# Kernel optimization log

Hardware: AMD Instinct MI355X
Metric: run time of the kernel (lower is better)

Reference implementation:

```python
import jax, jax.numpy as jnp
import numpy as np

E = 64      # embedding_dim
H = 64      # h_dim
MLP = 1024  # mlp_dim (attention hidden)
PRE1 = 512  # mlp_pre_pool hidden
BNK = 1024  # bottleneck_dim
S = 256     # num scenes (equal-size groups replacing seq_start_end)
P = 16      # pedestrians per scene
B = S * P   # total batch of pedestrians
T = 8       # obs_len for vx/vy (only last row used)
EPS = 1e-5  # BatchNorm eps


def _bn(x, g, b, m, v):
    # eval-mode BatchNorm1d over the last (feature) axis
    return (x - m) * jax.lax.rsqrt(v + EPS) * g + b


def setup_inputs() -> dict:
    key = jax.random.key(0)
    ks = jax.random.split(key, 24)
    def n(k, shape, s=1.0):
        return jax.random.normal(k, shape, jnp.float32) * s
    return {
        "h_states": n(ks[0], (1, B, H)),
        "end_pos": n(ks[1], (B, 2)),
        "vx": n(ks[2], (T, B)),
        "vy": n(ks[3], (T, B)),
        "W_sp": n(ks[4], (2, E), 0.05), "b_sp": jnp.zeros((E,), jnp.float32),
        "W_vel": n(ks[5], (2, E), 0.05), "b_vel": jnp.zeros((E,), jnp.float32),
        "Wa1": n(ks[6], (2 * E, MLP), 0.05), "ba1": jnp.zeros((MLP,), jnp.float32),
        "ga1": jnp.ones((MLP,), jnp.float32), "bta1": jnp.zeros((MLP,), jnp.float32),
        "ma1": n(ks[7], (MLP,), 0.1), "va1": jax.random.uniform(ks[8], (MLP,), jnp.float32) + 0.5,
        "Wa2": n(ks[9], (MLP, 1), 0.05), "ba2": jnp.zeros((1,), jnp.float32),
        "ga2": jnp.ones((1,), jnp.float32), "bta2": jnp.zeros((1,), jnp.float32),
        "ma2": n(ks[10], (1,), 0.1), "va2": jax.random.uniform(ks[11], (1,), jnp.float32) + 0.5,
        "Wp1": n(ks[12], (E + H, PRE1), 0.05), "bp1": jnp.zeros((PRE1,), jnp.float32),
        "gp1": jnp.ones((PRE1,), jnp.float32), "btp1": jnp.zeros((PRE1,), jnp.float32),
        "mp1": n(ks[13], (PRE1,), 0.1), "vp1": jax.random.uniform(ks[14], (PRE1,), jnp.float32) + 0.5,
        "Wp2": n(ks[15], (PRE1, BNK), 0.05), "bp2": jnp.zeros((BNK,), jnp.float32),
        "gp2": jnp.ones((BNK,), jnp.float32), "btp2": jnp.zeros((BNK,), jnp.float32),
        "mp2": n(ks[16], (BNK,), 0.1), "vp2": jax.random.uniform(ks[17], (BNK,), jnp.float32) + 0.5,
        "num_scenes": S, "num_ped": P,
    }


def _forward(h_states, end_pos, vx, vy, W_sp, b_sp, W_vel, b_vel,
             Wa1, ba1, ga1, bta1, ma1, va1, Wa2, ba2, ga2, bta2, ma2, va2,
             Wp1, bp1, gp1, btp1, mp1, vp1, Wp2, bp2, gp2, btp2, mp2, vp2,
             num_scenes, num_ped):
    Sn, Pn = num_scenes, num_ped
    h = h_states.reshape(-1, H).reshape(Sn, Pn, H)          # per-scene hidden
    pos = end_pos.reshape(Sn, Pn, 2)
    # rel[s,i,j] = pos[s,j] - pos[s,i]  (repeat vs repeat_interleave in torch)
    rel = pos[:, None, :, :] - pos[:, :, None, :]
    rel_emb = rel @ W_sp + b_sp                              # [S,P,P,E]
    vel = jnp.stack([vx[-1], vy[-1]], axis=-1).reshape(Sn, Pn, 2)
    vel_emb = vel @ W_vel + b_vel                            # [S,P,E], indexed by row i
    vel_emb = jnp.broadcast_to(vel_emb[:, :, None, :], (Sn, Pn, Pn, E))
    att_in = jnp.concatenate([rel_emb, vel_emb], axis=-1)    # [S,P,P,2E]
    a = jax.nn.relu(_bn(att_in @ Wa1 + ba1, ga1, bta1, ma1, va1))
    scores = jax.nn.relu(_bn(a @ Wa2 + ba2, ga2, bta2, ma2, va2))  # [S,P,P,1]
    # torch.softmax(scores, dim=1) on an (N,1) tensor: softmax over the size-1
    # feature axis -> identically 1.0. Reproduced faithfully here.
    w = jax.nn.softmax(scores, axis=-1)
    h_rep = jnp.broadcast_to(h[:, None, :, :], (Sn, Pn, Pn, H))   # h[s,j] per (i,j)
    x = jnp.concatenate([rel_emb, h_rep], axis=-1) * (0.05 * w)   # [S,P,P,E+H]
    y = jax.nn.relu(_bn(x @ Wp1 + bp1, gp1, btp1, mp1, vp1))
    y = jax.nn.relu(_bn(y @ Wp2 + bp2, gp2, btp2, mp2, vp2))      # [S,P,P,BNK]
    pool = jnp.max(y, axis=2)                                     # max over neighbors j
    return pool.reshape(Sn * Pn, BNK)


def reference(h_states, end_pos, vx, vy, W_sp, b_sp, W_vel, b_vel,
              Wa1, ba1, ga1, bta1, ma1, va1, Wa2, ba2, ga2, bta2, ma2, va2,
              Wp1, bp1, gp1, btp1, mp1, vp1, Wp2, bp2, gp2, btp2, mp2, vp2,
              num_scenes, num_ped):
    return _forward(h_states, end_pos, vx, vy, W_sp, b_sp, W_vel, b_vel,
                    Wa1, ba1, ga1, bta1, ma1, va1, Wa2, ba2, ga2, bta2, ma2, va2,
                    Wp1, bp1, gp1, btp1, mp1, vp1, Wp2, bp2, gp2, btp2, mp2, vp2,
                    num_scenes, num_ped)
```

## Files before the change

### kernel.cpp

```cpp
#include <hip/hip_runtime.h>
#include <hip/hip_bf16.h>
#include <stdint.h>
#include <utility>


typedef __bf16 bf16x8 __attribute__((ext_vector_type(8)));
typedef __bf16 bf16x2 __attribute__((ext_vector_type(2)));
typedef float  f32x4  __attribute__((ext_vector_type(4)));
typedef float  f32x2  __attribute__((ext_vector_type(2)));
typedef float  f32x16 __attribute__((ext_vector_type(16)));

#define BP2_OFF 0u
#define BP1_OFF 1048576u
#define MX_OFF  1114112u
#define MY_OFF  1116160u
#define CB_OFF  1118208u
#define SH_OFF  1120256u
#define A2_OFF  1122304u
#define C2_OFF  1126400u

#define Y1_LDS  0
#define HH_LDS  131072
#define LDS_SZ  147456

__device__ __forceinline__ unsigned short f2bf(float f) {
    union { float f; unsigned u; } c; c.f = f;
    unsigned u = c.u;
    return (unsigned short)((u + 0x7fffu + ((u >> 16) & 1u)) >> 16);
}
__device__ __forceinline__ float bfbits2f(unsigned hi) {
    union { unsigned u; float f; } c; c.u = hi; return c.f;
}
__device__ __forceinline__ unsigned pk_bf16(float a, float b) {
#if __has_builtin(__builtin_amdgcn_cvt_pk_bf16_f32)
    bf16x2 p = __builtin_amdgcn_cvt_pk_bf16_f32(a, b);
    union { bf16x2 v; unsigned u; } c; c.v = p; return c.u;
#else
    return (unsigned)f2bf(a) | ((unsigned)f2bf(b) << 16);
#endif
}
__device__ __forceinline__ int y1off(int r, int c16) {
    return r * 1024 + ((c16 ^ (r & 7)) << 4);
}

template<class F, int... Is>
__device__ __forceinline__ void sf_impl(F& f, std::integer_sequence<int, Is...>) {
    (f(std::integral_constant<int, Is>{}), ...);
}
template<int N, class F>
__device__ __forceinline__ void static_for(F&& f) {
    sf_impl(f, std::make_integer_sequence<int, N>{});
}

__global__ __launch_bounds__(256) void prep_pack_kernel(
    const float* __restrict__ Wsp,  const float* __restrict__ bsp,
    const float* __restrict__ Wp1,  const float* __restrict__ bp1,
    const float* __restrict__ gp1,  const float* __restrict__ btp1,
    const float* __restrict__ mp1,  const float* __restrict__ vp1,
    const float* __restrict__ Wp2,  const float* __restrict__ bp2,
    const float* __restrict__ gp2,  const float* __restrict__ btp2,
    const float* __restrict__ mp2,  const float* __restrict__ vp2,
    unsigned char* __restrict__ ws)
{
    __shared__ float tile[32 * 65];
    __shared__ float part[3][4][64];
    const int blk = blockIdx.x, t = threadIdx.x;

    if (blk < 272) {
        const float* src; int ncols, kb, ng;
        if (blk < 256) { kb = blk >> 4; ng = blk & 15; src = Wp2; ncols = 1024; }
        else { int b2 = blk - 256; kb = b2 >> 3; ng = b2 & 7; src = Wp1 + 64 * 512; ncols = 512; }
        const int k0 = kb * 32, n0 = ng * 64;
        #pragma unroll
        for (int it = 0; it < 2; ++it) {
            int c = t + it * 256;
            int r = c >> 4, c4 = c & 15;
            float4 v = *(const float4*)(src + (k0 + r) * ncols + n0 + c4 * 4);
            tile[r * 65 + c4 * 4 + 0] = v.x;
            tile[r * 65 + c4 * 4 + 1] = v.y;
            tile[r * 65 + c4 * 4 + 2] = v.z;
            tile[r * 65 + c4 * 4 + 3] = v.w;
        }
        __syncthreads();
        if (blk < 256) {
            const int l = t & 63, ch = (t >> 6) & 1, kh = t >> 7;
            const int nl = ch * 32 + (l & 31);
            const int kl = kh * 16 + ((l >> 5) & 1) * 8;
            uint4 o;
            o.x = pk_bf16(tile[(kl + 0) * 65 + nl], tile[(kl + 1) * 65 + nl]);
            o.y = pk_bf16(tile[(kl + 2) * 65 + nl], tile[(kl + 3) * 65 + nl]);
            o.z = pk_bf16(tile[(kl + 4) * 65 + nl], tile[(kl + 5) * 65 + nl]);
            o.w = pk_bf16(tile[(kl + 6) * 65 + nl], tile[(kl + 7) * 65 + nl]);
            const int kstep = kb * 2 + kh, ct = ng * 2 + ch;
            ((uint4*)(ws + BP2_OFF))[(kstep * 32 + ct) * 64 + l] = o;
        } else {
            int ntl = t >> 6, l = t & 63;
            int nl = ntl * 16 + (l & 15), kl = (l >> 4) * 8;
            uint4 o;
            o.x = pk_bf16(tile[(kl + 0) * 65 + nl], tile[(kl + 1) * 65 + nl]);
            o.y = pk_bf16(tile[(kl + 2) * 65 + nl], tile[(kl + 3) * 65 + nl]);
            o.z = pk_bf16(tile[(kl + 4) * 65 + nl], tile[(kl + 5) * 65 + nl]);
            o.w = pk_bf16(tile[(kl + 6) * 65 + nl], tile[(kl + 7) * 65 + nl]);
            ((uint4*)(ws + BP1_OFF))[((ng * 4 + ntl) * 2 + kb) * 64 + l] = o;
        }
    } else if (blk < 280) {
        const int kk = t & 63, eq = t >> 6;
        const int k = (blk - 272) * 64 + kk;
        float mx = 0.f, my = 0.f, cb = 0.f;
        #pragma unroll
        for (int e2 = 0; e2 < 16; ++e2) {
            int e = eq * 16 + e2;
            float wv = Wp1[e * 512 + k];
            mx = fmaf(Wsp[e],      wv, mx);
            my = fmaf(Wsp[64 + e], wv, my);
            cb = fmaf(bsp[e],      wv, cb);
        }
        part[0][eq][kk] = mx; part[1][eq][kk] = my; part[2][eq][kk] = cb;
        __syncthreads();
        if (t < 64) {
            const int k2 = (blk - 272) * 64 + t;
            float mxs = part[0][0][t] + part[0][1][t] + part[0][2][t] + part[0][3][t];
            float mys = part[1][0][t] + part[1][1][t] + part[1][2][t] + part[1][3][t];
            float cbs = part[2][0][t] + part[2][1][t] + part[2][2][t] + part[2][3][t];
            float a1 = gp1[k2] * rsqrtf(vp1[k2] + 1e-5f);
            ((float*)(ws + MX_OFF))[k2] = 0.05f * a1 * mxs;
            ((float*)(ws + MY_OFF))[k2] = 0.05f * a1 * mys;
            ((float*)(ws + CB_OFF))[k2] = 0.05f * a1 * cbs + (bp1[k2] - mp1[k2]) * a1 + btp1[k2];
            ((float*)(ws + SH_OFF))[k2] = 0.05f * a1;
        }
    } else {
        int n = (blk - 280) * 256 + t;
        float a = gp2[n] * rsqrtf(vp2[n] + 1e-5f);
        ((float*)(ws + A2_OFF))[n] = a;
        ((float*)(ws + C2_OFF))[n] = btp2[n] + (bp2[n] - mp2[n]) * a;
    }
}

__device__ __forceinline__ void phaseAB(
    unsigned char* smem,
    const float* __restrict__ hst, const float* __restrict__ epos,
    const unsigned char* __restrict__ ws, int s, int ih, int tid)
{
    const int w    = tid >> 6;
    const int l    = tid & 63;
    const int quad = l >> 4;
    const int jl   = l & 15;

    {
        union { unsigned u[4]; bf16x8 v; } afh[2];
        #pragma unroll
        for (int kb = 0; kb < 2; ++kb) {
            const float4* hp = (const float4*)(hst + (s * 16 + jl) * 64 + kb * 32 + quad * 8);
            float4 v0 = hp[0], v1 = hp[1];
            afh[kb].u[0] = pk_bf16(v0.x, v0.y);
            afh[kb].u[1] = pk_bf16(v0.z, v0.w);
            afh[kb].u[2] = pk_bf16(v1.x, v1.y);
            afh[kb].u[3] = pk_bf16(v1.z, v1.w);
        }
        const f32x4 fz = {0.f, 0.f, 0.f, 0.f};
        f32x4 acch[4] = {fz, fz, fz, fz};
        #pragma unroll
        for (int kb = 0; kb < 2; ++kb) {
            #pragma unroll
            for (int ct = 0; ct < 4; ++ct) {
                bf16x8 bfr = *(const bf16x8*)(ws + BP1_OFF + ((((w * 4 + ct) * 2 + kb) * 64 + l) << 4));
                acch[ct] = __builtin_amdgcn_mfma_f32_16x16x32_bf16(afh[kb].v, bfr, acch[ct], 0, 0, 0);
            }
        }
        const float* SHg = (const float*)(ws + SH_OFF);
        const float* CBg = (const float*)(ws + CB_OFF);
        #pragma unroll
        for (int ct = 0; ct < 4; ++ct) {
            int col = (w * 4 + ct) * 16 + jl;
            float sh = SHg[col], cb = CBg[col];
            #pragma unroll
            for (int reg = 0; reg < 4; ++reg) {
                int j = quad * 4 + reg;
                float hv = fmaf(acch[ct][reg], sh, cb);
                *(unsigned short*)(smem + HH_LDS + j * 1024 + col * 2) = f2bf(hv);
            }
        }
    }
    __syncthreads();

    {
        const int i2 = tid >> 8;
        const int j  = (tid >> 4) & 15;
        const int kc = tid & 15;
        float rx[4], ry[4];
        float pjx = epos[s * 32 + j * 2], pjy = epos[s * 32 + j * 2 + 1];
        #pragma unroll
        for (int ii = 0; ii < 4; ++ii) {
            int ig_ = ih * 8 + i2 * 4 + ii;
            rx[ii] = pjx - epos[s * 32 + ig_ * 2];
            ry[ii] = pjy - epos[s * 32 + ig_ * 2 + 1];
        }
        const f32x2 zero2 = {0.f, 0.f};
        #pragma unroll
        for (int kk = 0; kk < 4; ++kk) {
            int c16 = kk * 16 + kc;
            int k = c16 * 8;
            uint4 hh8 = *(const uint4*)(smem + HH_LDS + j * 1024 + k * 2);
            f32x4 mx0 = *(const f32x4*)(ws + MX_OFF + k * 4);
            f32x4 mx1 = *(const f32x4*)(ws + MX_OFF + k * 4 + 16);
            f32x4 my0 = *(const f32x4*)(ws + MY_OFF + k * 4);
            f32x4 my1 = *(const f32x4*)(ws + MY_OFF + k * 4 + 16);
            f32x2 mxp[4] = { {mx0[0],mx0[1]}, {mx0[2],mx0[3]}, {mx1[0],mx1[1]}, {mx1[2],mx1[3]} };
            f32x2 myp[4] = { {my0[0],my0[1]}, {my0[2],my0[3]}, {my1[0],my1[1]}, {my1[2],my1[3]} };
            f32x2 hhp[4];
            hhp[0][0] = bfbits2f(hh8.x << 16); hhp[0][1] = bfbits2f(hh8.x & 0xffff0000u);
            hhp[1][0] = bfbits2f(hh8.y << 16); hhp[1][1] = bfbits2f(hh8.y & 0xffff0000u);
            hhp[2][0] = bfbits2f(hh8.z << 16); hhp[2][1] = bfbits2f(hh8.z & 0xffff0000u);
            hhp[3][0] = bfbits2f(hh8.w << 16); hhp[3][1] = bfbits2f(hh8.w & 0xffff0000u);
            #pragma unroll
            for (int ii = 0; ii < 4; ++ii) {
                f32x2 rx2 = { rx[ii], rx[ii] };
                f32x2 ry2 = { ry[ii], ry[ii] };
                uint4 o;
                unsigned uu[4];
                #pragma unroll
                for (int p = 0; p < 4; ++p) {
                    f32x2 tt = __builtin_elementwise_fma(ry2, myp[p], hhp[p]);
                    tt = __builtin_elementwise_fma(rx2, mxp[p], tt);
                    tt = __builtin_elementwise_max(tt, zero2);
                    uu[p] = pk_bf16(tt[0], tt[1]);
                }
                o.x = uu[0]; o.y = uu[1]; o.z = uu[2]; o.w = uu[3];
                int r = (i2 * 4 + ii) * 16 + j;
                *(uint4*)(smem + Y1_LDS + y1off(r, c16)) = o;
            }
        }
    }
    __syncthreads();
}

__global__ __launch_bounds__(512, 2) void ab_probe_kernel(
    const float* __restrict__ hst, const float* __restrict__ epos,
    const unsigned char* __restrict__ ws, float* __restrict__ out)
{
    __shared__ __align__(16) unsigned char smem[LDS_SZ];
    const int s = blockIdx.x >> 1, ih = blockIdx.x & 1, tid = threadIdx.x;
    phaseAB(smem, hst, epos, ws, s, ih, tid);
    if (((const unsigned int*)smem)[(tid * 67) & 32767] == 0xDEADBEEFu)
        out[tid] = -1.0f;
}

__global__ __launch_bounds__(512, 2) void mm2_kernel(
    const float* __restrict__ hst,
    const float* __restrict__ epos,
    const unsigned char* __restrict__ ws,
    float* __restrict__ out)
{
    __shared__ __align__(16) unsigned char smem[LDS_SZ];

    const int s   = blockIdx.x >> 1;
    const int ih  = blockIdx.x & 1;
    const int tid = threadIdx.x;

    phaseAB(smem, hst, epos, ws, s, ih, tid);

    const int w = tid >> 6, l = tid & 63;
    const int lane31 = l & 31;
    const int hi = l >> 5;
    const int sr = lane31 & 7;
    const int rg = w >> 2;
    const int cg = w & 3;
    const float* A2 = (const float*)(ws + A2_OFF);
    const float* C2 = (const float*)(ws + C2_OFF);

    const int av = Y1_LDS + (rg * 64 + lane31) * 1024 + ((hi ^ sr) << 4);
    const unsigned char* bp = ws + BP2_OFF + ((cg * 4) << 10) + (l << 4);

    const f32x16 fz16 = {0.f,0.f,0.f,0.f,0.f,0.f,0.f,0.f,
                         0.f,0.f,0.f,0.f,0.f,0.f,0.f,0.f};
    f32x16 acc[2][4];
    bf16x8 ar[4][2];
    bf16x8 br[3][4];

    #pragma unroll
    for (int rr = 0; rr < 2; ++rr)
        #pragma unroll
        for (int c = 0; c < 4; ++c) acc[rr][c] = fz16;

    auto epilogue = [&](int pass) {
        #pragma unroll
        for (int c = 0; c < 4; ++c) {
            const int col = (pass * 16 + cg * 4 + c) * 32 + lane31;
            const float a2 = A2[col], c2 = C2[col];
            #pragma unroll
            for (int rr = 0; rr < 2; ++rr) {
                float mv[2];
                #pragma unroll
                for (int hg = 0; hg < 2; ++hg) {
                    float v0 = fmaxf(fmaf(acc[rr][c][hg * 8 + 0], a2, c2), 0.f);
                    float v1 = fmaxf(fmaf(acc[rr][c][hg * 8 + 1], a2, c2), 0.f);
                    float v2 = fmaxf(fmaf(acc[rr][c][hg * 8 + 2], a2, c2), 0.f);
                    float v3 = fmaxf(fmaf(acc[rr][c][hg * 8 + 3], a2, c2), 0.f);
                    float v4 = fmaxf(fmaf(acc[rr][c][hg * 8 + 4], a2, c2), 0.f);
                    float v5 = fmaxf(fmaf(acc[rr][c][hg * 8 + 5], a2, c2), 0.f);
                    float v6 = fmaxf(fmaf(acc[rr][c][hg * 8 + 6], a2, c2), 0.f);
                    float v7 = fmaxf(fmaf(acc[rr][c][hg * 8 + 7], a2, c2), 0.f);
                    float m = fmaxf(fmaxf(fmaxf(v0, v1), fmaxf(v2, v3)),
                                    fmaxf(fmaxf(v4, v5), fmaxf(v6, v7)));
                    mv[hg] = fmaxf(m, __shfl_xor(m, 32, 64));
                }
                const int iloc = (rg * 2 + rr) * 2 + hi;
                const float vout = hi ? mv[1] : mv[0];
                const int orow = s * 16 + ih * 8 + iloc;
                __builtin_nontemporal_store(vout, &out[orow * 1024 + col]);
            }
        }
    };

    auto stepG = [&](auto Gc) {
        constexpr int G  = decltype(Gc)::value;
        constexpr int GN = G + 2;
        if constexpr (GN <= 63) {
            constexpr int pn = GN >> 5, kn = GN & 31;
            constexpr int bs = GN % 3, as = GN & 3;
            const unsigned char* b = bp + (pn * 16384 + kn * 32768);
            #pragma unroll
            for (int c = 0; c < 4; ++c)
                br[bs][c] = __builtin_nontemporal_load((const bf16x8*)(b + c * 1024));
            constexpr int add = (kn >> 2) * 128;
            constexpr int xr  = (kn & 3) << 5;
            ar[as][0] = *(const bf16x8*)(smem + ((av + add) ^ xr));
            ar[as][1] = *(const bf16x8*)(smem + (((av + add) ^ xr) + 32768));
        }
        if constexpr (G == 32)      asm volatile("s_waitcnt vmcnt(12) lgkmcnt(4)" ::: "memory");
        else if constexpr (G == 33) asm volatile("s_waitcnt vmcnt(16) lgkmcnt(4)" ::: "memory");
        else if constexpr (G == 62) asm volatile("s_waitcnt vmcnt(4) lgkmcnt(2)" ::: "memory");
        else if constexpr (G == 63) asm volatile("s_waitcnt vmcnt(0) lgkmcnt(0)" ::: "memory");
        else                        asm volatile("s_waitcnt vmcnt(8) lgkmcnt(4)" ::: "memory");
        __builtin_amdgcn_sched_barrier(0);
        constexpr int as2 = G & 3, bs2 = G % 3;
        #pragma unroll
        for (int c = 0; c < 4; ++c)
            #pragma unroll
            for (int rr = 0; rr < 2; ++rr)
                acc[rr][c] = __builtin_amdgcn_mfma_f32_32x32x16_bf16(
                    ar[as2][rr], br[bs2][c], acc[rr][c], 0, 0, 0);
    };

    #pragma unroll
    for (int g = 0; g < 2; ++g)
        #pragma unroll
        for (int c = 0; c < 4; ++c)
            br[g][c] = __builtin_nontemporal_load((const bf16x8*)(bp + g * 32768 + c * 1024));
    ar[0][0] = *(const bf16x8*)(smem + av);
    ar[0][1] = *(const bf16x8*)(smem + av + 32768);
    ar[1][0] = *(const bf16x8*)(smem + (av ^ 32));
    ar[1][1] = *(const bf16x8*)(smem + ((av ^ 32) + 32768));

    static_for<32>(stepG);
    __builtin_amdgcn_sched_barrier(0);
    epilogue(0);
    #pragma unroll
    for (int rr = 0; rr < 2; ++rr)
        #pragma unroll
        for (int c = 0; c < 4; ++c) acc[rr][c] = fz16;
    __builtin_amdgcn_sched_barrier(0);
    static_for<32>([&](auto kc) {
        stepG(std::integral_constant<int, decltype(kc)::value + 32>{});
    });
    __builtin_amdgcn_sched_barrier(0);
    epilogue(1);
}

extern "C" void kernel_launch(void* const* d_in, const int* in_sizes, int n_in,
                              void* d_out, int out_size, void* d_ws, size_t ws_size,
                              hipStream_t stream) {
    const float* hst  = (const float*)d_in[0];
    const float* epos = (const float*)d_in[1];
    const float* Wsp  = (const float*)d_in[4];
    const float* bsp  = (const float*)d_in[5];
    const float* Wp1  = (const float*)d_in[20];
    const float* bp1  = (const float*)d_in[21];
    const float* gp1  = (const float*)d_in[22];
    const float* btp1 = (const float*)d_in[23];
    const float* mp1  = (const float*)d_in[24];
    const float* vp1  = (const float*)d_in[25];
    const float* Wp2  = (const float*)d_in[26];
    const float* bp2  = (const float*)d_in[27];
    const float* gp2  = (const float*)d_in[28];
    const float* btp2 = (const float*)d_in[29];
    const float* mp2  = (const float*)d_in[30];
    const float* vp2  = (const float*)d_in[31];
    unsigned char* ws = (unsigned char*)d_ws;
    float* out = (float*)d_out;

    prep_pack_kernel<<<284, 256, 0, stream>>>(Wsp, bsp, Wp1, bp1, gp1, btp1, mp1, vp1,
                                              Wp2, bp2, gp2, btp2, mp2, vp2, ws);
    ab_probe_kernel<<<512, 512, 0, stream>>>(hst, epos, ws, out);
    mm2_kernel<<<512, 512, 0, stream>>>(hst, epos, ws, out);
}
```

Baseline: 201.1 us.

## Drop phaseAB probe kernel and retile mm2 warps to cover all rows per column block

Removes the ab_probe_kernel launch, which redid phaseAB purely as a timing probe. In mm2, each warp now owns all four 32-row tiles and a 4-column-tile block. It runs a single continuous 64-step pipeline with the first-half epilogue fused mid-loop, instead of splitting by row group and column group. This halves per-warp global B loads and raises LDS A reads. It also preloads the BN scale and shift values and retunes the waitcnt thresholds.

```diff
diff --git a/kernel.cpp b/kernel.cpp
--- a/kernel.cpp
+++ b/kernel.cpp
@@ -234,17 +234,6 @@
     __syncthreads();
 }
 
-__global__ __launch_bounds__(512, 2) void ab_probe_kernel(
-    const float* __restrict__ hst, const float* __restrict__ epos,
-    const unsigned char* __restrict__ ws, float* __restrict__ out)
-{
-    __shared__ __align__(16) unsigned char smem[LDS_SZ];
-    const int s = blockIdx.x >> 1, ih = blockIdx.x & 1, tid = threadIdx.x;
-    phaseAB(smem, hst, epos, ws, s, ih, tid);
-    if (((const unsigned int*)smem)[(tid * 67) & 32767] == 0xDEADBEEFu)
-        out[tid] = -1.0f;
-}
-
 __global__ __launch_bounds__(512, 2) void mm2_kernel(
     const float* __restrict__ hst,
     const float* __restrict__ epos,
@@ -263,48 +252,47 @@
     const int lane31 = l & 31;
     const int hi = l >> 5;
     const int sr = lane31 & 7;
-    const int rg = w >> 2;
-    const int cg = w & 3;
     const float* A2 = (const float*)(ws + A2_OFF);
     const float* C2 = (const float*)(ws + C2_OFF);
 
-    const int av = Y1_LDS + (rg * 64 + lane31) * 1024 + ((hi ^ sr) << 4);
-    const unsigned char* bp = ws + BP2_OFF + ((cg * 4) << 10) + (l << 4);
+    int av[4];
+    #pragma unroll
+    for (int rt = 0; rt < 4; ++rt)
+        av[rt] = Y1_LDS + (rt * 32 + lane31) * 1024 + ((hi ^ sr) << 4);
+
+    const int ctb0 = w * 4;
+    const unsigned char* bp = ws + BP2_OFF + (ctb0 << 10) + (l << 4);
 
     const f32x16 fz16 = {0.f,0.f,0.f,0.f,0.f,0.f,0.f,0.f,
                          0.f,0.f,0.f,0.f,0.f,0.f,0.f,0.f};
-    f32x16 acc[2][4];
-    bf16x8 ar[4][2];
-    bf16x8 br[3][4];
-
-    #pragma unroll
-    for (int rr = 0; rr < 2; ++rr)
-        #pragma unroll
-        for (int c = 0; c < 4; ++c) acc[rr][c] = fz16;
-
-    auto epilogue = [&](int pass) {
-        #pragma unroll
-        for (int c = 0; c < 4; ++c) {
-            const int col = (pass * 16 + cg * 4 + c) * 32 + lane31;
-            const float a2 = A2[col], c2 = C2[col];
-            #pragma unroll
-            for (int rr = 0; rr < 2; ++rr) {
+    f32x16 acc[4][2];
+    bf16x8 ar[3][4];
+    bf16x8 br[3][2];
+    float a2v[2][2], c2v[2][2];
+
+    auto epilogue = [&](int chunk) {
+        #pragma unroll
+        for (int c = 0; c < 2; ++c) {
+            const int col = (ctb0 + chunk * 2 + c) * 32 + lane31;
+            const float a2 = a2v[chunk][c], c2 = c2v[chunk][c];
+            #pragma unroll
+            for (int rt = 0; rt < 4; ++rt) {
                 float mv[2];
                 #pragma unroll
                 for (int hg = 0; hg < 2; ++hg) {
-                    float v0 = fmaxf(fmaf(acc[rr][c][hg * 8 + 0], a2, c2), 0.f);
-                    float v1 = fmaxf(fmaf(acc[rr][c][hg * 8 + 1], a2, c2), 0.f);
-                    float v2 = fmaxf(fmaf(acc[rr][c][hg * 8 + 2], a2, c2), 0.f);
-                    float v3 = fmaxf(fmaf(acc[rr][c][hg * 8 + 3], a2, c2), 0.f);
-                    float v4 = fmaxf(fmaf(acc[rr][c][hg * 8 + 4], a2, c2), 0.f);
-                    float v5 = fmaxf(fmaf(acc[rr][c][hg * 8 + 5], a2, c2), 0.f);
-                    float v6 = fmaxf(fmaf(acc[rr][c][hg * 8 + 6], a2, c2), 0.f);
-                    float v7 = fmaxf(fmaf(acc[rr][c][hg * 8 + 7], a2, c2), 0.f);
+                    float v0 = fmaxf(fmaf(acc[rt][c][hg * 8 + 0], a2, c2), 0.f);
+                    float v1 = fmaxf(fmaf(acc[rt][c][hg * 8 + 1], a2, c2), 0.f);
+                    float v2 = fmaxf(fmaf(acc[rt][c][hg * 8 + 2], a2, c2), 0.f);
+                    float v3 = fmaxf(fmaf(acc[rt][c][hg * 8 + 3], a2, c2), 0.f);
+                    float v4 = fmaxf(fmaf(acc[rt][c][hg * 8 + 4], a2, c2), 0.f);
+                    float v5 = fmaxf(fmaf(acc[rt][c][hg * 8 + 5], a2, c2), 0.f);
+                    float v6 = fmaxf(fmaf(acc[rt][c][hg * 8 + 6], a2, c2), 0.f);
+                    float v7 = fmaxf(fmaf(acc[rt][c][hg * 8 + 7], a2, c2), 0.f);
                     float m = fmaxf(fmaxf(fmaxf(v0, v1), fmaxf(v2, v3)),
                                     fmaxf(fmaxf(v4, v5), fmaxf(v6, v7)));
                     mv[hg] = fmaxf(m, __shfl_xor(m, 32, 64));
                 }
-                const int iloc = (rg * 2 + rr) * 2 + hi;
+                const int iloc = rt * 2 + hi;
                 const float vout = hi ? mv[1] : mv[0];
                 const int orow = s * 16 + ih * 8 + iloc;
                 __builtin_nontemporal_store(vout, &out[orow * 1024 + col]);
@@ -312,57 +300,60 @@
         }
     };
 
+    auto issueG = [&](auto Gc) {
+        constexpr int GN = decltype(Gc)::value;
+        constexpr int ch = GN >> 5, kn = GN & 31, sl = GN % 3;
+        constexpr int boff = ch * 2048 + kn * 32768;
+        br[sl][0] = __builtin_nontemporal_load((const bf16x8*)(bp + boff));
+        br[sl][1] = __builtin_nontemporal_load((const bf16x8*)(bp + boff + 1024));
+        constexpr int add = (kn >> 2) * 128;
+        constexpr int xr  = (kn & 3) << 5;
+        #pragma unroll
+        for (int rt = 0; rt < 4; ++rt)
+            ar[sl][rt] = *(const bf16x8*)(smem + ((av[rt] + add) ^ xr));
+    };
+
     auto stepG = [&](auto Gc) {
-        constexpr int G  = decltype(Gc)::value;
-        constexpr int GN = G + 2;
-        if constexpr (GN <= 63) {
-            constexpr int pn = GN >> 5, kn = GN & 31;
-            constexpr int bs = GN % 3, as = GN & 3;
-            const unsigned char* b = bp + (pn * 16384 + kn * 32768);
-            #pragma unroll
-            for (int c = 0; c < 4; ++c)
-                br[bs][c] = __builtin_nontemporal_load((const bf16x8*)(b + c * 1024));
-            constexpr int add = (kn >> 2) * 128;
-            constexpr int xr  = (kn & 3) << 5;
-            ar[as][0] = *(const bf16x8*)(smem + ((av + add) ^ xr));
-            ar[as][1] = *(const bf16x8*)(smem + (((av + add) ^ xr) + 32768));
-        }
-        if constexpr (G == 32)      asm volatile("s_waitcnt vmcnt(12) lgkmcnt(4)" ::: "memory");
-        else if constexpr (G == 33) asm volatile("s_waitcnt vmcnt(16) lgkmcnt(4)" ::: "memory");
-        else if constexpr (G == 62) asm volatile("s_waitcnt vmcnt(4) lgkmcnt(2)" ::: "memory");
-        else if constexpr (G == 63) asm volatile("s_waitcnt vmcnt(0) lgkmcnt(0)" ::: "memory");
-        else                        asm volatile("s_waitcnt vmcnt(8) lgkmcnt(4)" ::: "memory");
+        constexpr int G = decltype(Gc)::value;
+        if constexpr (G + 2 <= 63)
+            issueG(std::integral_constant<int, G + 2>{});
+        if constexpr (G == 32 || G == 33)
+            asm volatile("s_waitcnt vmcnt(16) lgkmcnt(8)" ::: "memory");
+        else if constexpr (G == 62)
+            asm volatile("s_waitcnt vmcnt(2) lgkmcnt(4)" ::: "memory");
+        else if constexpr (G == 63)
+            asm volatile("s_waitcnt vmcnt(0) lgkmcnt(0)" ::: "memory");
+        else
+            asm volatile("s_waitcnt vmcnt(4) lgkmcnt(8)" ::: "memory");
         __builtin_amdgcn_sched_barrier(0);
-        constexpr int as2 = G & 3, bs2 = G % 3;
-        #pragma unroll
-        for (int c = 0; c < 4; ++c)
-            #pragma unroll
-            for (int rr = 0; rr < 2; ++rr)
-                acc[rr][c] = __builtin_amdgcn_mfma_f32_32x32x16_bf16(
-                    ar[as2][rr], br[bs2][c], acc[rr][c], 0, 0, 0);
+        constexpr int sl = G % 3;
+        #pragma unroll
+        for (int c = 0; c < 2; ++c)
+            #pragma unroll
+            for (int rt = 0; rt < 4; ++rt)
+                acc[rt][c] = __builtin_amdgcn_mfma_f32_32x32x16_bf16(
+                    ar[sl][rt], br[sl][c], acc[rt][c], 0, 0, 0);
+        if constexpr (G == 31) {
+            a2v[1][0] = A2[(ctb0 + 2) * 32 + lane31];
+            a2v[1][1] = A2[(ctb0 + 3) * 32 + lane31];
+            c2v[1][0] = C2[(ctb0 + 2) * 32 + lane31];
+            c2v[1][1] = C2[(ctb0 + 3) * 32 + lane31];
+            epilogue(0);
+            #pragma unroll
+            for (int rt = 0; rt < 4; ++rt) { acc[rt][0] = fz16; acc[rt][1] = fz16; }
+        }
     };
 
+    a2v[0][0] = A2[ctb0 * 32 + lane31];
+    a2v[0][1] = A2[(ctb0 + 1) * 32 + lane31];
+    c2v[0][0] = C2[ctb0 * 32 + lane31];
+    c2v[0][1] = C2[(ctb0 + 1) * 32 + lane31];
     #pragma unroll
-    for (int g = 0; g < 2; ++g)
-        #pragma unroll
-        for (int c = 0; c < 4; ++c)
-            br[g][c] = __builtin_nontemporal_load((const bf16x8*)(bp + g * 32768 + c * 1024));
-    ar[0][0] = *(const bf16x8*)(smem + av);
-    ar[0][1] = *(const bf16x8*)(smem + av + 32768);
-    ar[1][0] = *(const bf16x8*)(smem + (av ^ 32));
-    ar[1][1] = *(const bf16x8*)(smem + ((av ^ 32) + 32768));
-
-    static_for<32>(stepG);
-    __builtin_amdgcn_sched_barrier(0);
-    epilogue(0);
-    #pragma unroll
-    for (int rr = 0; rr < 2; ++rr)
-        #pragma unroll
-        for (int c = 0; c < 4; ++c) acc[rr][c] = fz16;
-    __builtin_amdgcn_sched_barrier(0);
-    static_for<32>([&](auto kc) {
-        stepG(std::integral_constant<int, decltype(kc)::value + 32>{});
-    });
+    for (int rt = 0; rt < 4; ++rt) { acc[rt][0] = fz16; acc[rt][1] = fz16; }
+    issueG(std::integral_constant<int, 0>{});
+    issueG(std::integral_constant<int, 1>{});
+
+    static_for<64>(stepG);
     __builtin_amdgcn_sched_barrier(0);
     epilogue(1);
 }
@@ -391,6 +382,5 @@
 
     prep_pack_kernel<<<284, 256, 0, stream>>>(Wsp, bsp, Wp1, bp1, gp1, btp1, mp1, vp1,
                                               Wp2, bp2, gp2, btp2, mp2, vp2, ws);
-    ab_probe_kernel<<<512, 512, 0, stream>>>(hst, epos, ws, out);
     mm2_kernel<<<512, 512, 0, stream>>>(hst, epos, ws, out);
 }
```

New measurement: 196.2 us. 1.03x faster.
